# Kernel tuning notes

Measured on AMD Instinct MI355X. Metric: run time of the kernel, lower is better.

Reference implementation:

```python
import jax, jax.numpy as jnp
import numpy as np
import heapq
from collections import defaultdict

N_PER, N_BATCH, C = 100000, 2, 128  # nodes per graph, num graphs, feature dim
TARGET = 50000                      # target node count per graph


def _build_graph():
    # Symmetric degree-4 ring graph per batch (offsets +/-1, +/-2), required so
    # neighbours[] lookups in the collapse algorithm never miss.
    within = np.tile(np.arange(N_PER), N_BATCH)
    base = np.repeat(np.arange(N_BATCH) * N_PER, N_PER)
    src_all, dst_all = [], []
    for o in (1, 2, -1, -2):
        src_all.append(base + within)
        dst_all.append(base + (within + o) % N_PER)
    ei = np.stack([np.concatenate(src_all), np.concatenate(dst_all)]).astype(np.int64)
    batch = np.repeat(np.arange(N_BATCH), N_PER).astype(np.int64)
    return ei, batch


def _collapse(x, edge_index, target_edge_count, batch):
    # Faithful port of the sequential heap-driven greedy collapse.
    N = x.shape[0]
    collapse_mask = np.ones(N, dtype=bool)
    x_mask = np.ones(N, dtype=bool)
    neighbours = defaultdict(list)
    for f, t in zip(edge_index[0].tolist(), edge_index[1].tolist()):
        neighbours[f].append(t)
    for batch_id in range(int(batch.max()) + 1):
        node_ids = np.nonzero(batch == batch_id)[0]
        num_nodes = int(node_ids.shape[0])
        mags = (x[node_ids] * x[node_ids]).sum(axis=1)  # squared magnitude priority
        heap = [[float(m), int(n)] for m, n in zip(mags, node_ids)]
        heapq.heapify(heap)
        while num_nodes > target_edge_count:
            if len(heap) == 0:
                break
            _, node_id = heapq.heappop(heap)
            node_id = int(node_id)
            if not collapse_mask[node_id]:
                continue
            collapse_mask[node_id] = False
            neighbour_ids = neighbours[node_id]
            num_nodes -= 1
            new_neighbour_ids = []
            for nb in neighbour_ids:
                x_mask[nb] = False
                collapse_mask[nb] = False
                num_nodes -= 1
                for nbnb in neighbours[nb]:
                    if nbnb in neighbour_ids or nbnb == node_id:
                        continue
                    new_neighbour_ids.append(nbnb)
                    neighbours[nbnb] = [n for n in neighbours[nbnb] if n != nb]
                    neighbours[nbnb].append(node_id)
            neighbours[node_id] = new_neighbour_ids
    # Remap surviving nodes to compact ids and rebuild edge_index.
    old_to_new = -np.ones(N, dtype=np.int64)
    new_to_old = np.nonzero(x_mask)[0]
    old_to_new[new_to_old] = np.arange(new_to_old.shape[0])
    rows, cols = [], []
    for new_id, old_id in enumerate(new_to_old.tolist()):
        for nid in neighbours[old_id]:
            rows.append(new_id)
            cols.append(int(old_to_new[nid]))
    new_ei = np.array([rows, cols], dtype=np.int64)
    return x_mask, new_ei


def setup_inputs() -> dict:
    key = jax.random.key(0)
    ei, batch = _build_graph()
    x = jax.random.normal(key, (N_BATCH * N_PER, C), dtype=jnp.float32)
    return {
        "x": x,
        "edge_index": jnp.asarray(ei),
        "target_edge_count": TARGET,
        "batch": jnp.asarray(batch),
        "vertices": jnp.zeros((1,), dtype=jnp.int32),
        "edges": jnp.zeros((1,), dtype=jnp.int32),
    }


def reference(x, edge_index, target_edge_count, batch, vertices, edges):
    # vertices/edges are unused by the original forward.
    x_mask, new_ei = _collapse(
        np.asarray(x), np.asarray(edge_index), int(target_edge_count), np.asarray(batch)
    )
    keep = jnp.asarray(np.nonzero(x_mask)[0])
    return x[keep], jnp.asarray(new_ei), batch[keep]
```

## Files before the change

### kernel.cpp

```cpp
#include <hip/hip_runtime.h>
#include <stdint.h>

#define N_PER   100000
#define N_TOT   200000
#define C_DIM   128
#define PAD     131072
#define NBLK    782
#define CMW     ((N_PER + 31) / 32)
#define MAXL    512
#define CANDMAX 2048

typedef unsigned long long u64;

__device__ __forceinline__ float mag128(const float4* __restrict__ p4) {
  float4 u = p4[0], v = p4[1];
  float r0 = __fmul_rn(u.x,u.x), r1 = __fmul_rn(u.y,u.y),
        r2 = __fmul_rn(u.z,u.z), r3 = __fmul_rn(u.w,u.w),
        r4 = __fmul_rn(v.x,v.x), r5 = __fmul_rn(v.y,v.y),
        r6 = __fmul_rn(v.z,v.z), r7 = __fmul_rn(v.w,v.w);
  #pragma unroll
  for (int m = 1; m < 16; ++m) {
    u = p4[2*m]; v = p4[2*m+1];
    r0 = __fadd_rn(r0, __fmul_rn(u.x,u.x));
    r1 = __fadd_rn(r1, __fmul_rn(u.y,u.y));
    r2 = __fadd_rn(r2, __fmul_rn(u.z,u.z));
    r3 = __fadd_rn(r3, __fmul_rn(u.w,u.w));
    r4 = __fadd_rn(r4, __fmul_rn(v.x,v.x));
    r5 = __fadd_rn(r5, __fmul_rn(v.y,v.y));
    r6 = __fadd_rn(r6, __fmul_rn(v.z,v.z));
    r7 = __fadd_rn(r7, __fmul_rn(v.w,v.w));
  }
  return __fadd_rn(__fadd_rn(__fadd_rn(r0,r1), __fadd_rn(r2,r3)),
                   __fadd_rn(__fadd_rn(r4,r5), __fadd_rn(r6,r7)));
}

__global__ void k_init_keys(const float* __restrict__ x, u64* __restrict__ keys) {
  int slot = blockIdx.x*blockDim.x + threadIdx.x;
  if (slot >= 2*PAD) return;
  int b = slot >> 17;
  int w = slot & (PAD-1);
  if (w < N_PER) {
    int node = b*N_PER + w;
    float mag = mag128((const float4*)(x + (size_t)node*C_DIM));
    keys[slot] = ((u64)__float_as_uint(mag) << 32) | (uint32_t)node;
  } else {
    keys[slot] = ~0ull;
  }
}

__global__ void k_init_graph(int* __restrict__ nbr, uint8_t* __restrict__ xm, int cap) {
  int node = blockIdx.x*blockDim.x + threadIdx.x;
  if (node >= N_TOT) return;
  int base = (node >= N_PER) ? N_PER : 0;
  int w = node - base;
  int* Lp = nbr + (size_t)node*cap;
  Lp[0] = 4;
  Lp[1] = base + (w + 1) % N_PER;
  Lp[2] = base + (w + 2) % N_PER;
  Lp[3] = base + (w + N_PER - 1) % N_PER;
  Lp[4] = base + (w + N_PER - 2) % N_PER;
  xm[node] = 1;
}

__global__ void k_bitonic(u64* __restrict__ keys, int k, int j) {
  int i = blockIdx.x*blockDim.x + threadIdx.x;
  if (i >= 2*PAD) return;
  int ixj = i ^ j;
  if (ixj <= i) return;
  int wi = i & (PAD-1);
  bool asc = ((wi & k) == 0);
  u64 a = keys[i], b = keys[ixj];
  bool sw = asc ? (a > b) : (a < b);
  if (sw) { keys[i] = b; keys[ixj] = a; }
}

__global__ __launch_bounds__(64) void k_collapse(const u64* __restrict__ keys,
                                                 int* __restrict__ nbr,
                                                 uint8_t* __restrict__ xm,
                                                 const int* __restrict__ tgt_p,
                                                 int cap) {
  __shared__ uint32_t s_cm[CMW];
  __shared__ int      s_mem[4][MAXL];
  __shared__ int      s_memlen[4];
  __shared__ int      s_cand[CANDMAX];
  __shared__ uint8_t  s_cg[CANDMAX];
  __shared__ int      s_node[MAXL];
  __shared__ int      s_final[MAXL];

  const int b    = blockIdx.x;
  const int lane = threadIdx.x;
  const int TGT  = tgt_p[0];
  const u64* ord = keys + (size_t)b * PAD;
  const int gbase = b * N_PER;
  const int g = lane >> 4, j = lane & 15;

  for (int w = lane; w < CMW; w += 64) s_cm[w] = 0xffffffffu;
  __syncthreads();

  int num_nodes = N_PER;
  for (int base2 = 0; base2 < N_PER && num_nodes > TGT; base2 += 64) {
    int nd_l = (int)(uint32_t)(ord[base2 + lane]);
    bool alive = false;
    if (base2 + lane < N_PER) {
      int locl = nd_l - gbase;
      alive = ((s_cm[locl >> 5] >> (locl & 31)) & 1u) != 0u;
    }
    u64 mask = __ballot(alive);
    while (mask != 0ull && num_nodes > TGT) {
      int k2 = __ffsll(mask) - 1;
      mask &= mask - 1;
      int node  = __shfl(nd_l, k2);
      int local = node - gbase;
      if (((s_cm[local >> 5] >> (local & 31)) & 1u) == 0u) continue;
      if (lane == 0) atomicAnd(&s_cm[local >> 5], ~(1u << (local & 31)));

      int* nodeL = nbr + (size_t)node * cap;
      int4 h0 = *(const int4*)nodeL;
      int  e3 = nodeL[4];
      int  L  = h0.x;

      if (L <= 4) {
        if (lane == 0) { s_node[0]=h0.y; s_node[1]=h0.z; s_node[2]=h0.w; s_node[3]=e3; }
      } else {
        for (int i = lane; i < L; i += 64) s_node[i] = nodeL[1 + i];
      }
      __syncthreads();

      for (int i = lane; i < L; i += 64) {
        int mv = s_node[i];
        xm[mv] = 0;
        int ml = mv - gbase;
        atomicAnd(&s_cm[ml >> 5], ~(1u << (ml & 31)));
      }
      num_nodes -= 1 + L;
      int mreg = (lane < L) ? s_node[lane] : -1;

      int Ctot = 0;
      for (int mc = 0; mc < L; mc += 4) {
        int Lc = (L - mc < 4) ? (L - mc) : 4;
        int m0 = s_node[mc];
        int m1 = (Lc > 1) ? s_node[mc+1] : -1;
        int m2 = (Lc > 2) ? s_node[mc+2] : -1;
        int m3 = (Lc > 3) ? s_node[mc+3] : -1;

        int mg = (g == 0) ? m0 : (g == 1) ? m1 : (g == 2) ? m2 : m3;
        const int* tlg = nbr + (size_t)mg * cap;
        if (g < Lc) {
          int4 c0 = *(const int4*)(tlg + 4*j);
          if (j == 0) s_memlen[g] = c0.x;
          if (j > 0)  s_mem[g][4*j - 1] = c0.x;
          s_mem[g][4*j + 0] = c0.y;
          s_mem[g][4*j + 1] = c0.z;
          s_mem[g][4*j + 2] = c0.w;
        }
        __syncthreads();
        int lg = (g < Lc) ? s_memlen[g] : 0;
        for (int s0 = 64 + 4*j; s0 <= lg; s0 += 64) {
          int4 cv = *(const int4*)(tlg + s0);
          s_mem[g][s0 - 1] = cv.x;
          if (s0 + 1 <= lg) s_mem[g][s0 + 0] = cv.y;
          if (s0 + 2 <= lg) s_mem[g][s0 + 1] = cv.z;
          if (s0 + 3 <= lg) s_mem[g][s0 + 2] = cv.w;
        }
        __syncthreads();

        int len0 = (Lc > 0) ? s_memlen[0] : 0;
        int len1 = (Lc > 1) ? s_memlen[1] : 0;
        int len2 = (Lc > 2) ? s_memlen[2] : 0;
        int len3 = (Lc > 3) ? s_memlen[3] : 0;
        int o1 = len0, o2 = o1 + len1, o3 = o2 + len2, T = o3 + len3;
        int C = 0;
        int LM = (L < 64) ? L : 64;
        for (int cb = 0; cb < T; cb += 64) {
          int i = cb + lane;
          bool act = i < T;
          int val = -1; int ggi = 0;
          if (act) {
            ggi = (i >= o1) + (i >= o2) + (i >= o3);
            int qb = (ggi == 0) ? 0 : (ggi == 1) ? o1 : (ggi == 2) ? o2 : o3;
            val = s_mem[ggi][i - qb];
          }
          bool ism = (val == node);
          for (int m = 0; m < LM; ++m) ism |= (val == __shfl(mreg, m));
          for (int i2 = 64; i2 < L; ++i2) ism |= (val == s_node[i2]);
          bool keep = act && !ism;
          u64 mk = __ballot(keep);
          if (keep) {
            int pos = C + __popcll(mk & ((1ull << lane) - 1ull));
            s_cand[pos] = val;
            s_cg[pos]   = (uint8_t)ggi;
          }
          C += __popcll(mk);
        }
        __syncthreads();

        for (int cb = 0; cb < C; cb += 64) {
          int c = cb + lane;
          bool own = (c < C);
          int val = own ? s_cand[c] : -1;
          if (own) {
            for (int p = 0; p < c; ++p)
              if (s_cand[p] == val) { own = false; break; }
          }
          if (own) {
            uint32_t rmg = 0; int kocc = 0;
            for (int p = c; p < C; ++p)
              if (s_cand[p] == val) { rmg |= 1u << s_cg[p]; ++kocc; }
            bool u0 = (rmg & 1u) != 0, u1 = (rmg & 2u) != 0,
                 u2 = (rmg & 4u) != 0, u3 = (rmg & 8u) != 0;
            int* tl = nbr + (size_t)val * cap;
            int L3 = tl[0];
            int wslot = 1;
            int nch = (L3 + 4) >> 2;
            for (int ch = 0; ch < nch; ++ch) {
              int4 v = *(const int4*)(tl + 4*ch);
              int s = 4*ch;
              if (s >= 1 && s <= L3) { int e = v.x;
                if (!((u0&&e==m0)||(u1&&e==m1)||(u2&&e==m2)||(u3&&e==m3))) tl[wslot++] = e; }
              if (s + 1 <= L3)       { int e = v.y;
                if (!((u0&&e==m0)||(u1&&e==m1)||(u2&&e==m2)||(u3&&e==m3))) tl[wslot++] = e; }
              if (s + 2 <= L3)       { int e = v.z;
                if (!((u0&&e==m0)||(u1&&e==m1)||(u2&&e==m2)||(u3&&e==m3))) tl[wslot++] = e; }
              if (s + 3 <= L3)       { int e = v.w;
                if (!((u0&&e==m0)||(u1&&e==m1)||(u2&&e==m2)||(u3&&e==m3))) tl[wslot++] = e; }
            }
            int fin = wslot - 1 + kocc;
            if (fin > cap - 1) fin = cap - 1;
            for (int a = wslot; a <= fin; ++a) tl[a] = node;
            tl[0] = fin;
          }
        }

        for (int k3 = lane; k3 < C; k3 += 64) {
          int gp = Ctot + k3;
          if (gp < cap - 1) s_final[gp] = s_cand[k3];
        }
        Ctot += C;
        __threadfence_block();
        __syncthreads();
      }

      int wl = (Ctot < cap - 1) ? Ctot : (cap - 1);
      if (lane == 0) nodeL[0] = wl;
      for (int k3 = lane; k3 < wl; k3 += 64) nodeL[1 + k3] = s_final[k3];
      __threadfence_block();
      __syncthreads();
    }
  }
}

__device__ __forceinline__ u64 pack_node(const uint8_t* xm, const int* nbr, int i, int cap) {
  int keep = xm[i];
  int el = keep ? nbr[(size_t)i*cap] : 0;
  return ((u64)(uint32_t)el << 32) | (uint32_t)keep;
}

__global__ void k_scan1(const uint8_t* __restrict__ xm, const int* __restrict__ nbr,
                        u64* __restrict__ bsum, int cap) {
  __shared__ u64 s[256];
  int t = threadIdx.x;
  int i = blockIdx.x*256 + t;
  u64 v = (i < N_TOT) ? pack_node(xm, nbr, i, cap) : 0ull;
  s[t] = v; __syncthreads();
  for (int off = 128; off > 0; off >>= 1) {
    if (t < off) s[t] += s[t+off];
    __syncthreads();
  }
  if (t == 0) bsum[blockIdx.x] = s[0];
}

__global__ void k_scan2(u64* __restrict__ bsum, int* __restrict__ cnt) {
  __shared__ u64 s[1024];
  int t = threadIdx.x;
  u64 v = (t < NBLK) ? bsum[t] : 0ull;
  s[t] = v; __syncthreads();
  for (int off = 1; off < 1024; off <<= 1) {
    u64 a = (t >= off) ? s[t-off] : 0ull;
    __syncthreads();
    s[t] += a;
    __syncthreads();
  }
  if (t < NBLK) bsum[t] = s[t] - v;
  if (t == 1023) {
    cnt[0] = (int)(s[1023] & 0xffffffffull);
    cnt[1] = (int)(s[1023] >> 32);
  }
}

__global__ void k_scan3(const uint8_t* __restrict__ xm, const int* __restrict__ nbr,
                        const u64* __restrict__ bsum,
                        int* __restrict__ newid, int* __restrict__ eoff, int cap) {
  __shared__ u64 s[256];
  int t = threadIdx.x;
  int i = blockIdx.x*256 + t;
  u64 v = (i < N_TOT) ? pack_node(xm, nbr, i, cap) : 0ull;
  s[t] = v; __syncthreads();
  for (int off = 1; off < 256; off <<= 1) {
    u64 a = (t >= off) ? s[t-off] : 0ull;
    __syncthreads();
    s[t] += a;
    __syncthreads();
  }
  u64 excl = s[t] - v + bsum[blockIdx.x];
  if (i < N_TOT) {
    newid[i] = (int)(excl & 0xffffffffull);
    eoff[i]  = (int)(excl >> 32);
  }
}

__global__ void k_write_x(const float* __restrict__ x, const uint8_t* __restrict__ xm,
                          const int* __restrict__ newid, float* __restrict__ out) {
  int tid = blockIdx.x*blockDim.x + threadIdx.x;
  int node = tid >> 5, q = tid & 31;
  if (node >= N_TOT || !xm[node]) return;
  const float4* src = (const float4*)(x + (size_t)node*C_DIM);
  float4* dst = (float4*)(out + (size_t)newid[node]*C_DIM);
  dst[q] = src[q];
}

__global__ __launch_bounds__(64) void k_write_edges(const uint8_t* __restrict__ xm,
                              const int* __restrict__ nbr,
                              const int* __restrict__ newid, const int* __restrict__ eoff,
                              const int* __restrict__ cnt, float* __restrict__ out, int cap) {
  int node = blockIdx.x;
  int lane = threadIdx.x;
  if (!xm[node]) return;
  int K = cnt[0], E = cnt[1];
  size_t base = (size_t)K * C_DIM;
  int nid = newid[node];
  if (lane == 0) out[base + 2*(size_t)E + nid] = (node >= N_PER) ? 1.0f : 0.0f;
  int len = nbr[(size_t)node*cap];
  int eo = eoff[node];
  for (int j = lane; j < len; j += 64) {
    int ent = nbr[(size_t)node*cap + 1 + j];
    int off = eo + j;
    out[base + off]             = (float)nid;
    out[base + (size_t)E + off] = xm[ent] ? (float)newid[ent] : -1.0f;
  }
}

extern "C" void kernel_launch(void* const* d_in, const int* in_sizes, int n_in,
                              void* d_out, int out_size, void* d_ws, size_t ws_size,
                              hipStream_t stream) {
  const float* x   = (const float*)d_in[0];
  const int*   tgt = (const int*)d_in[2];
  float* out = (float*)d_out;
  uint8_t* ws = (uint8_t*)d_ws;

  size_t off = 0;
  auto alloc = [&](size_t bytes) -> void* {
    void* p = ws + off;
    off += (bytes + 255) & ~(size_t)255;
    return p;
  };
  u64*     keys  = (u64*)alloc((size_t)2*PAD*8);
  uint8_t* xm    = (uint8_t*)alloc(N_TOT);
  int*     newid = (int*)alloc((size_t)N_TOT*4);
  int*     eoff  = (int*)alloc((size_t)N_TOT*4);
  u64*     bsum  = (u64*)alloc((size_t)1024*8);
  int*     cnt   = (int*)alloc(256);
  size_t remain = (ws_size > off + 64) ? (ws_size - off - 64) : 0;
  int cap = (int)(remain / ((size_t)N_TOT * 4));
  cap &= ~3;
  if (cap > 512) cap = 512;
  if (cap < 68)  cap = 68;
  int* nbr = (int*)(ws + off);

  k_init_keys<<<(2*PAD)/256, 256, 0, stream>>>(x, keys);
  k_init_graph<<<NBLK, 256, 0, stream>>>(nbr, xm, cap);

  for (int k = 2; k <= PAD; k <<= 1)
    for (int j = k >> 1; j >= 1; j >>= 1)
      k_bitonic<<<(2*PAD)/256, 256, 0, stream>>>(keys, k, j);

  k_collapse<<<2, 64, 0, stream>>>(keys, nbr, xm, tgt, cap);

  k_scan1<<<NBLK, 256, 0, stream>>>(xm, nbr, bsum, cap);
  k_scan2<<<1, 1024, 0, stream>>>(bsum, cnt);
  k_scan3<<<NBLK, 256, 0, stream>>>(xm, nbr, bsum, newid, eoff, cap);

  k_write_x<<<(N_TOT*32)/256, 256, 0, stream>>>(x, xm, newid, out);
  k_write_edges<<<N_TOT, 64, 0, stream>>>(xm, nbr, newid, eoff, cnt, out, cap);
}
```

Measured before the change: 42.31 ms.

## Speculatively batch up to four heap pops per iteration with conflict detection

The collapse loop now collects up to four live candidate nodes at a time. It loads their neighbour rows and second-hop rows together, then computes each candidate's new neighbour list in parallel. A sequential check accepts candidates until one conflicts with an earlier accepted one or has overflowed its buffer, and commits the accepted ones in a single merged update pass. The goal is to cut the per-pop serial latency of global loads and barriers, at the cost of much more shared memory, complex conflict checks, and rollback of the scan position. Overflowing candidates fall back to the old single-node path.

```diff
diff --git a/kernel.cpp b/kernel.cpp
--- a/kernel.cpp
+++ b/kernel.cpp
@@ -9,6 +9,7 @@
 #define CMW     ((N_PER + 31) / 32)
 #define MAXL    512
 #define CANDMAX 2048
+#define W       4
 
 typedef unsigned long long u64;
 
@@ -80,134 +81,319 @@
                                                  const int* __restrict__ tgt_p,
                                                  int cap) {
   __shared__ uint32_t s_cm[CMW];
-  __shared__ int      s_mem[4][MAXL];
-  __shared__ int      s_memlen[4];
-  __shared__ int      s_cand[CANDMAX];
-  __shared__ uint8_t  s_cg[CANDMAX];
-  __shared__ int      s_node[MAXL];
-  __shared__ int      s_final[MAXL];
+  __shared__ int      s_prow[W][MAXL];
+  __shared__ int      s_mem[4*W][MAXL];
+  __shared__ int      s_memlen[4*W];
+  __shared__ int      s_cand[W][CANDMAX];
+  __shared__ uint16_t s_cg[W][CANDMAX];
+  __shared__ int      s_fin[MAXL];
+  __shared__ int      s_pop[W], s_plenB[W], s_Cc[W], s_ovf[W];
+  __shared__ int      s_gb2[W];
+  __shared__ u64      s_gmask[W];
 
   const int b    = blockIdx.x;
   const int lane = threadIdx.x;
   const int TGT  = tgt_p[0];
   const u64* ord = keys + (size_t)b * PAD;
   const int gbase = b * N_PER;
-  const int g = lane >> 4, j = lane & 15;
 
   for (int w = lane; w < CMW; w += 64) s_cm[w] = 0xffffffffu;
   __syncthreads();
 
   int num_nodes = N_PER;
-  for (int base2 = 0; base2 < N_PER && num_nodes > TGT; base2 += 64) {
-    int nd_l = (int)(uint32_t)(ord[base2 + lane]);
-    bool alive = false;
-    if (base2 + lane < N_PER) {
-      int locl = nd_l - gbase;
-      alive = ((s_cm[locl >> 5] >> (locl & 31)) & 1u) != 0u;
+  int base2 = -64;
+  u64 mask = 0ull;
+  int nd_l = -1;
+
+  while (num_nodes > TGT) {
+    int Wp = 0;
+    for (;;) {
+      if (Wp >= W) break;
+      if (mask == 0ull) {
+        base2 += 64;
+        if (base2 >= N_PER) break;
+        nd_l = (base2 + lane < N_PER) ? (int)(uint32_t)ord[base2 + lane] : -1;
+        bool av = false;
+        if (base2 + lane < N_PER) {
+          int ll = nd_l - gbase;
+          av = ((s_cm[ll>>5] >> (ll&31)) & 1u) != 0u;
+        }
+        mask = __ballot(av);
+        continue;
+      }
+      if (lane == 0) { s_gb2[Wp] = base2; s_gmask[Wp] = mask; }
+      int k2 = __ffsll((long long)mask) - 1;
+      mask &= mask - 1ull;
+      int node = __shfl(nd_l, k2);
+      int ll = node - gbase;
+      if (((s_cm[ll>>5] >> (ll&31)) & 1u) == 0u) continue;
+      if (lane == 0) s_pop[Wp] = node;
+      ++Wp;
     }
-    u64 mask = __ballot(alive);
-    while (mask != 0ull && num_nodes > TGT) {
-      int k2 = __ffsll(mask) - 1;
-      mask &= mask - 1;
-      int node  = __shfl(nd_l, k2);
-      int local = node - gbase;
-      if (((s_cm[local >> 5] >> (local & 31)) & 1u) == 0u) continue;
-      if (lane == 0) atomicAnd(&s_cm[local >> 5], ~(1u << (local & 31)));
-
+    __syncthreads();
+    if (Wp == 0) break;
+
+    {
+      int p = lane >> 4, jj = lane & 15;
+      const int* rowp = nullptr;
+      if (p < Wp) {
+        rowp = nbr + (size_t)s_pop[p] * cap;
+        int4 c0 = *(const int4*)(rowp + 4*jj);
+        if (jj == 0) s_plenB[p] = c0.x;
+        else         s_prow[p][4*jj - 1] = c0.x;
+        s_prow[p][4*jj + 0] = c0.y;
+        s_prow[p][4*jj + 1] = c0.z;
+        s_prow[p][4*jj + 2] = c0.w;
+      }
+      __syncthreads();
+      if (p < Wp) {
+        int lg = s_plenB[p];
+        for (int s0 = 64 + 4*jj; s0 <= lg; s0 += 64) {
+          int4 cv = *(const int4*)(rowp + s0);
+          s_prow[p][s0 - 1] = cv.x;
+          if (s0 + 1 <= lg) s_prow[p][s0 + 0] = cv.y;
+          if (s0 + 2 <= lg) s_prow[p][s0 + 1] = cv.z;
+          if (s0 + 3 <= lg) s_prow[p][s0 + 2] = cv.w;
+        }
+      }
+      __syncthreads();
+    }
+
+    {
+      int r = lane >> 2, q4 = lane & 3;
+      int rp = r >> 2, rg = r & 3;
+      bool rOK = (rp < Wp) && (rg < s_plenB[rp]) && (rg < 4);
+      const int* tlg = nullptr;
+      if (rOK) {
+        int m = s_prow[rp][rg];
+        tlg = nbr + (size_t)m * cap;
+        int4 c0 = *(const int4*)(tlg + 4*q4);
+        if (q4 == 0) s_memlen[r] = c0.x;
+        else         s_mem[r][4*q4 - 1] = c0.x;
+        s_mem[r][4*q4 + 0] = c0.y;
+        s_mem[r][4*q4 + 1] = c0.z;
+        s_mem[r][4*q4 + 2] = c0.w;
+      }
+      __syncthreads();
+      if (rOK) {
+        int lg = s_memlen[r];
+        for (int s0 = 16 + 4*q4; s0 <= lg; s0 += 16) {
+          int4 cv = *(const int4*)(tlg + s0);
+          s_mem[r][s0 - 1] = cv.x;
+          if (s0 + 1 <= lg) s_mem[r][s0 + 0] = cv.y;
+          if (s0 + 2 <= lg) s_mem[r][s0 + 1] = cv.z;
+          if (s0 + 3 <= lg) s_mem[r][s0 + 2] = cv.w;
+        }
+      }
+      __syncthreads();
+    }
+
+    for (int p2 = 0; p2 < Wp; ++p2) {
+      int L = s_plenB[p2];
+      int node = s_pop[p2];
+      int C = 0, ovf = 0;
+      for (int mc = 0; mc < L; mc += 4) {
+        if (ovf) break;
+        int Lc = (L - mc < 4) ? (L - mc) : 4;
+        if (mc > 0) {
+          int g = lane >> 4, jj = lane & 15;
+          const int* tlg2 = nullptr;
+          if (g < Lc) {
+            int m = s_prow[p2][mc + g];
+            tlg2 = nbr + (size_t)m * cap;
+            int4 c0 = *(const int4*)(tlg2 + 4*jj);
+            if (jj == 0) s_memlen[4*p2 + g] = c0.x;
+            else         s_mem[4*p2 + g][4*jj - 1] = c0.x;
+            s_mem[4*p2 + g][4*jj + 0] = c0.y;
+            s_mem[4*p2 + g][4*jj + 1] = c0.z;
+            s_mem[4*p2 + g][4*jj + 2] = c0.w;
+          }
+          __syncthreads();
+          if (g < Lc) {
+            int lg = s_memlen[4*p2 + g];
+            for (int s0 = 64 + 4*jj; s0 <= lg; s0 += 64) {
+              int4 cv = *(const int4*)(tlg2 + s0);
+              s_mem[4*p2 + g][s0 - 1] = cv.x;
+              if (s0 + 1 <= lg) s_mem[4*p2 + g][s0 + 0] = cv.y;
+              if (s0 + 2 <= lg) s_mem[4*p2 + g][s0 + 1] = cv.z;
+              if (s0 + 3 <= lg) s_mem[4*p2 + g][s0 + 2] = cv.w;
+            }
+          }
+          __syncthreads();
+        }
+        int br = 4*p2;
+        int len0 = (Lc > 0) ? s_memlen[br+0] : 0;
+        int len1 = (Lc > 1) ? s_memlen[br+1] : 0;
+        int len2 = (Lc > 2) ? s_memlen[br+2] : 0;
+        int len3 = (Lc > 3) ? s_memlen[br+3] : 0;
+        int o1 = len0, o2 = o1 + len1, o3 = o2 + len2, T = o3 + len3;
+        for (int cb = 0; cb < T; cb += 64) {
+          int i = cb + lane;
+          bool act = i < T;
+          int val = -1, ggi = 0;
+          if (act) {
+            ggi = (i >= o1) + (i >= o2) + (i >= o3);
+            int qb = (ggi == 0) ? 0 : (ggi == 1) ? o1 : (ggi == 2) ? o2 : o3;
+            val = s_mem[br + ggi][i - qb];
+          }
+          bool ism = (val == node);
+          for (int t = 0; t < L; ++t) ism |= (val == s_prow[p2][t]);
+          bool keep = act && !ism;
+          u64 mk = __ballot(keep);
+          int cnt = __popcll(mk);
+          if (C + cnt > CANDMAX) { ovf = 1; break; }
+          if (keep) {
+            int pos = C + __popcll(mk & ((1ull << lane) - 1ull));
+            s_cand[p2][pos] = val;
+            s_cg[p2][pos]   = (uint16_t)(mc + ggi);
+          }
+          C += cnt;
+        }
+      }
+      if (lane == 0) { s_Cc[p2] = C; s_ovf[p2] = ovf; }
+      __syncthreads();
+    }
+
+    int statbits = 0;
+    int nn = num_nodes;
+    int consumed = Wp;
+    int solo = 0;
+    for (int jx = 0; jx < Wp; ++jx) {
+      if (nn <= TGT) { consumed = jx; break; }
+      int pj = s_pop[jx];
+      int Lj = s_plenB[jx];
+      bool dead = false;
+      for (int i = 0; i < jx && !dead; ++i) {
+        if (((statbits >> (2*i)) & 3) != 1) continue;
+        int Li = s_plenB[i];
+        for (int cb = 0; cb < Li && !dead; cb += 64) {
+          bool h = (cb + lane < Li) && (s_prow[i][cb + lane] == pj);
+          if (__ballot(h) != 0ull) dead = true;
+        }
+      }
+      if (dead) { statbits |= 2 << (2*jx); continue; }
+      if (s_ovf[jx]) {
+        if (jx == 0) { solo = 1; consumed = 1; }
+        else consumed = jx;
+        break;
+      }
+      bool conf = false;
+      for (int i = 0; i < jx && !conf; ++i) {
+        if (((statbits >> (2*i)) & 3) != 1) continue;
+        int pi = s_pop[i];
+        int Ci = s_Cc[i];
+        int Cj = s_Cc[jx];
+        for (int cb = 0; cb < Lj && !conf; cb += 64) {
+          bool h = (cb + lane < Lj) && (s_prow[jx][cb + lane] == pi);
+          if (__ballot(h) != 0ull) conf = true;
+        }
+        for (int cb = 0; cb < Cj && !conf; cb += 64) {
+          bool h = (cb + lane < Cj) && (s_cand[jx][cb + lane] == pi);
+          if (__ballot(h) != 0ull) conf = true;
+        }
+        for (int cb = 0; cb < Ci && !conf; cb += 64) {
+          int e = (cb + lane < Ci) ? s_cand[i][cb + lane] : -1;
+          bool h = false;
+          if (cb + lane < Ci) {
+            h = (e == pj);
+            for (int t = 0; t < Lj; ++t) h |= (e == s_prow[jx][t]);
+            for (int t = 0; t < Cj; ++t) h |= (e == s_cand[jx][t]);
+          }
+          if (__ballot(h) != 0ull) conf = true;
+        }
+      }
+      if (conf) { consumed = jx; break; }
+      statbits |= 1 << (2*jx);
+      nn -= 1 + Lj;
+    }
+
+    if (solo) {
+      int node = s_pop[0];
+      int L = s_plenB[0];
+      if (lane == 0) {
+        int ll = node - gbase;
+        atomicAnd(&s_cm[ll>>5], ~(1u << (ll&31)));
+      }
+      for (int t = lane; t < L; t += 64) {
+        int m = s_prow[0][t];
+        xm[m] = 0;
+        int ml = m - gbase;
+        atomicAnd(&s_cm[ml>>5], ~(1u << (ml&31)));
+      }
+      num_nodes -= 1 + L;
+      __syncthreads();
       int* nodeL = nbr + (size_t)node * cap;
-      int4 h0 = *(const int4*)nodeL;
-      int  e3 = nodeL[4];
-      int  L  = h0.x;
-
-      if (L <= 4) {
-        if (lane == 0) { s_node[0]=h0.y; s_node[1]=h0.z; s_node[2]=h0.w; s_node[3]=e3; }
-      } else {
-        for (int i = lane; i < L; i += 64) s_node[i] = nodeL[1 + i];
-      }
-      __syncthreads();
-
-      for (int i = lane; i < L; i += 64) {
-        int mv = s_node[i];
-        xm[mv] = 0;
-        int ml = mv - gbase;
-        atomicAnd(&s_cm[ml >> 5], ~(1u << (ml & 31)));
-      }
-      num_nodes -= 1 + L;
-      int mreg = (lane < L) ? s_node[lane] : -1;
-
       int Ctot = 0;
       for (int mc = 0; mc < L; mc += 4) {
         int Lc = (L - mc < 4) ? (L - mc) : 4;
-        int m0 = s_node[mc];
-        int m1 = (Lc > 1) ? s_node[mc+1] : -1;
-        int m2 = (Lc > 2) ? s_node[mc+2] : -1;
-        int m3 = (Lc > 3) ? s_node[mc+3] : -1;
-
-        int mg = (g == 0) ? m0 : (g == 1) ? m1 : (g == 2) ? m2 : m3;
-        const int* tlg = nbr + (size_t)mg * cap;
-        if (g < Lc) {
-          int4 c0 = *(const int4*)(tlg + 4*j);
-          if (j == 0) s_memlen[g] = c0.x;
-          if (j > 0)  s_mem[g][4*j - 1] = c0.x;
-          s_mem[g][4*j + 0] = c0.y;
-          s_mem[g][4*j + 1] = c0.z;
-          s_mem[g][4*j + 2] = c0.w;
-        }
-        __syncthreads();
-        int lg = (g < Lc) ? s_memlen[g] : 0;
-        for (int s0 = 64 + 4*j; s0 <= lg; s0 += 64) {
-          int4 cv = *(const int4*)(tlg + s0);
-          s_mem[g][s0 - 1] = cv.x;
-          if (s0 + 1 <= lg) s_mem[g][s0 + 0] = cv.y;
-          if (s0 + 2 <= lg) s_mem[g][s0 + 1] = cv.z;
-          if (s0 + 3 <= lg) s_mem[g][s0 + 2] = cv.w;
-        }
-        __syncthreads();
-
-        int len0 = (Lc > 0) ? s_memlen[0] : 0;
-        int len1 = (Lc > 1) ? s_memlen[1] : 0;
-        int len2 = (Lc > 2) ? s_memlen[2] : 0;
-        int len3 = (Lc > 3) ? s_memlen[3] : 0;
-        int o1 = len0, o2 = o1 + len1, o3 = o2 + len2, T = o3 + len3;
+        int m0 = s_prow[0][mc];
+        int m1 = (Lc > 1) ? s_prow[0][mc+1] : -1;
+        int m2 = (Lc > 2) ? s_prow[0][mc+2] : -1;
+        int m3 = (Lc > 3) ? s_prow[0][mc+3] : -1;
+        {
+          int g = lane >> 4, jj = lane & 15;
+          const int* tlg2 = nullptr;
+          if (g < Lc) {
+            int m = (g==0)?m0:(g==1)?m1:(g==2)?m2:m3;
+            tlg2 = nbr + (size_t)m * cap;
+            int4 c0 = *(const int4*)(tlg2 + 4*jj);
+            if (jj == 0) s_memlen[g] = c0.x;
+            else         s_mem[g][4*jj - 1] = c0.x;
+            s_mem[g][4*jj + 0] = c0.y;
+            s_mem[g][4*jj + 1] = c0.z;
+            s_mem[g][4*jj + 2] = c0.w;
+          }
+          __syncthreads();
+          if (g < Lc) {
+            int lg = s_memlen[g];
+            for (int s0 = 64 + 4*jj; s0 <= lg; s0 += 64) {
+              int4 cv = *(const int4*)(tlg2 + s0);
+              s_mem[g][s0 - 1] = cv.x;
+              if (s0 + 1 <= lg) s_mem[g][s0 + 0] = cv.y;
+              if (s0 + 2 <= lg) s_mem[g][s0 + 1] = cv.z;
+              if (s0 + 3 <= lg) s_mem[g][s0 + 2] = cv.w;
+            }
+          }
+          __syncthreads();
+        }
+        int len0=(Lc>0)?s_memlen[0]:0, len1=(Lc>1)?s_memlen[1]:0,
+            len2=(Lc>2)?s_memlen[2]:0, len3=(Lc>3)?s_memlen[3]:0;
+        int o1=len0, o2=o1+len1, o3=o2+len2, T=o3+len3;
         int C = 0;
-        int LM = (L < 64) ? L : 64;
         for (int cb = 0; cb < T; cb += 64) {
           int i = cb + lane;
           bool act = i < T;
-          int val = -1; int ggi = 0;
+          int val = -1, ggi = 0;
           if (act) {
             ggi = (i >= o1) + (i >= o2) + (i >= o3);
             int qb = (ggi == 0) ? 0 : (ggi == 1) ? o1 : (ggi == 2) ? o2 : o3;
             val = s_mem[ggi][i - qb];
           }
           bool ism = (val == node);
-          for (int m = 0; m < LM; ++m) ism |= (val == __shfl(mreg, m));
-          for (int i2 = 64; i2 < L; ++i2) ism |= (val == s_node[i2]);
+          for (int t = 0; t < L; ++t) ism |= (val == s_prow[0][t]);
           bool keep = act && !ism;
           u64 mk = __ballot(keep);
           if (keep) {
             int pos = C + __popcll(mk & ((1ull << lane) - 1ull));
-            s_cand[pos] = val;
-            s_cg[pos]   = (uint8_t)ggi;
+            s_cand[0][pos] = val;
+            s_cg[0][pos] = (uint16_t)ggi;
           }
           C += __popcll(mk);
         }
         __syncthreads();
-
         for (int cb = 0; cb < C; cb += 64) {
           int c = cb + lane;
           bool own = (c < C);
-          int val = own ? s_cand[c] : -1;
+          int val = own ? s_cand[0][c] : -1;
           if (own) {
             for (int p = 0; p < c; ++p)
-              if (s_cand[p] == val) { own = false; break; }
+              if (s_cand[0][p] == val) { own = false; break; }
           }
           if (own) {
             uint32_t rmg = 0; int kocc = 0;
             for (int p = c; p < C; ++p)
-              if (s_cand[p] == val) { rmg |= 1u << s_cg[p]; ++kocc; }
-            bool u0 = (rmg & 1u) != 0, u1 = (rmg & 2u) != 0,
-                 u2 = (rmg & 4u) != 0, u3 = (rmg & 8u) != 0;
+              if (s_cand[0][p] == val) { rmg |= 1u << s_cg[0][p]; ++kocc; }
+            bool u0=(rmg&1u)!=0, u1=(rmg&2u)!=0, u2=(rmg&4u)!=0, u3=(rmg&8u)!=0;
             int* tl = nbr + (size_t)val * cap;
             int L3 = tl[0];
             int wslot = 1;
@@ -215,14 +401,14 @@
             for (int ch = 0; ch < nch; ++ch) {
               int4 v = *(const int4*)(tl + 4*ch);
               int s = 4*ch;
-              if (s >= 1 && s <= L3) { int e = v.x;
-                if (!((u0&&e==m0)||(u1&&e==m1)||(u2&&e==m2)||(u3&&e==m3))) tl[wslot++] = e; }
-              if (s + 1 <= L3)       { int e = v.y;
-                if (!((u0&&e==m0)||(u1&&e==m1)||(u2&&e==m2)||(u3&&e==m3))) tl[wslot++] = e; }
-              if (s + 2 <= L3)       { int e = v.z;
-                if (!((u0&&e==m0)||(u1&&e==m1)||(u2&&e==m2)||(u3&&e==m3))) tl[wslot++] = e; }
-              if (s + 3 <= L3)       { int e = v.w;
-                if (!((u0&&e==m0)||(u1&&e==m1)||(u2&&e==m2)||(u3&&e==m3))) tl[wslot++] = e; }
+              if (s >= 1 && s <= L3) { int e=v.x;
+                if (!((u0&&e==m0)||(u1&&e==m1)||(u2&&e==m2)||(u3&&e==m3))) tl[wslot++]=e; }
+              if (s + 1 <= L3)       { int e=v.y;
+                if (!((u0&&e==m0)||(u1&&e==m1)||(u2&&e==m2)||(u3&&e==m3))) tl[wslot++]=e; }
+              if (s + 2 <= L3)       { int e=v.z;
+                if (!((u0&&e==m0)||(u1&&e==m1)||(u2&&e==m2)||(u3&&e==m3))) tl[wslot++]=e; }
+              if (s + 3 <= L3)       { int e=v.w;
+                if (!((u0&&e==m0)||(u1&&e==m1)||(u2&&e==m2)||(u3&&e==m3))) tl[wslot++]=e; }
             }
             int fin = wslot - 1 + kocc;
             if (fin > cap - 1) fin = cap - 1;
@@ -230,21 +416,108 @@
             tl[0] = fin;
           }
         }
-
         for (int k3 = lane; k3 < C; k3 += 64) {
           int gp = Ctot + k3;
-          if (gp < cap - 1) s_final[gp] = s_cand[k3];
+          if (gp < cap - 1) s_fin[gp] = s_cand[0][k3];
         }
         Ctot += C;
         __threadfence_block();
         __syncthreads();
       }
-
       int wl = (Ctot < cap - 1) ? Ctot : (cap - 1);
       if (lane == 0) nodeL[0] = wl;
-      for (int k3 = lane; k3 < wl; k3 += 64) nodeL[1 + k3] = s_final[k3];
+      for (int k3 = lane; k3 < wl; k3 += 64) nodeL[1 + k3] = s_fin[k3];
       __threadfence_block();
       __syncthreads();
+    } else {
+      for (int p3 = 0; p3 < Wp; ++p3) {
+        if (((statbits >> (2*p3)) & 3) != 1) continue;
+        int node = s_pop[p3];
+        int L = s_plenB[p3];
+        int* nodeL = nbr + (size_t)node * cap;
+        if (lane == 0) {
+          int ll = node - gbase;
+          atomicAnd(&s_cm[ll>>5], ~(1u << (ll&31)));
+        }
+        for (int t = lane; t < L; t += 64) {
+          int m = s_prow[p3][t];
+          xm[m] = 0;
+          int ml = m - gbase;
+          atomicAnd(&s_cm[ml>>5], ~(1u << (ml&31)));
+        }
+        int C = s_Cc[p3];
+        int wl = (C < cap - 1) ? C : (cap - 1);
+        if (lane == 0) nodeL[0] = wl;
+        for (int t = lane; t < wl; t += 64) nodeL[1 + t] = s_cand[p3][t];
+      }
+      int C0p = (((statbits >> 0) & 3) == 1) ? s_Cc[0] : 0;
+      int C1p = (Wp > 1 && ((statbits >> 2) & 3) == 1) ? s_Cc[1] : 0;
+      int C2p = (Wp > 2 && ((statbits >> 4) & 3) == 1) ? s_Cc[2] : 0;
+      int C3p = (Wp > 3 && ((statbits >> 6) & 3) == 1) ? s_Cc[3] : 0;
+      int tot = C0p + C1p + C2p + C3p;
+      for (int cb = 0; cb < tot; cb += 64) {
+        int idx = cb + lane;
+        bool act = idx < tot;
+        int c = idx, p = 0;
+        if (act) {
+          if (c >= C0p) { c -= C0p; p = 1;
+            if (c >= C1p) { c -= C1p; p = 2;
+              if (c >= C2p) { c -= C2p; p = 3; } } }
+        }
+        int Cp = (p == 0) ? C0p : (p == 1) ? C1p : (p == 2) ? C2p : C3p;
+        int val = act ? s_cand[p][c] : -1;
+        bool own = act;
+        if (own) {
+          for (int q = 0; q < c; ++q)
+            if (s_cand[p][q] == val) { own = false; break; }
+        }
+        if (own) {
+          int node = s_pop[p];
+          int kocc = 0;
+          for (int q = c; q < Cp; ++q) if (s_cand[p][q] == val) ++kocc;
+          auto rem = [&](int e) -> bool {
+            for (int q = c; q < Cp; ++q)
+              if (s_cand[p][q] == val && s_prow[p][(int)s_cg[p][q]] == e) return true;
+            return false;
+          };
+          int* tl = nbr + (size_t)val * cap;
+          int4 v0 = *(const int4*)tl;
+          int4 v1 = *(const int4*)(tl + 4);
+          int L3 = v0.x;
+          int wslot = 1;
+          if (L3 >= 1) { int e=v0.y; if (!rem(e)) tl[wslot++]=e; }
+          if (L3 >= 2) { int e=v0.z; if (!rem(e)) tl[wslot++]=e; }
+          if (L3 >= 3) { int e=v0.w; if (!rem(e)) tl[wslot++]=e; }
+          if (L3 >= 4) { int e=v1.x; if (!rem(e)) tl[wslot++]=e; }
+          if (L3 >= 5) { int e=v1.y; if (!rem(e)) tl[wslot++]=e; }
+          if (L3 >= 6) { int e=v1.z; if (!rem(e)) tl[wslot++]=e; }
+          if (L3 >= 7) { int e=v1.w; if (!rem(e)) tl[wslot++]=e; }
+          for (int s0 = 8; s0 <= L3; s0 += 4) {
+            int4 v = *(const int4*)(tl + s0);
+            { int e=v.x;                 if (!rem(e)) tl[wslot++]=e; }
+            if (s0 + 1 <= L3) { int e=v.y; if (!rem(e)) tl[wslot++]=e; }
+            if (s0 + 2 <= L3) { int e=v.z; if (!rem(e)) tl[wslot++]=e; }
+            if (s0 + 3 <= L3) { int e=v.w; if (!rem(e)) tl[wslot++]=e; }
+          }
+          int fin = wslot - 1 + kocc;
+          if (fin > cap - 1) fin = cap - 1;
+          for (int a = wslot; a <= fin; ++a) tl[a] = node;
+          tl[0] = fin;
+        }
+      }
+      num_nodes = nn;
+      __threadfence_block();
+      __syncthreads();
+    }
+
+    if (consumed < Wp) {
+      int nb2 = s_gb2[consumed];
+      u64 nmask = s_gmask[consumed];
+      if (nb2 != base2) {
+        base2 = nb2;
+        nd_l = (base2 + lane < N_PER) ? (int)(uint32_t)ord[base2 + lane] : -1;
+      }
+      mask = nmask;
     }
   }
 }
```

After: 53.84 ms. 27.2% more time.

## Prefetch next alive node's adjacency row and use shared bitmask for member tests

Applied to the files above, without the earlier changes.

Inside the sequential collapse kernel, the next alive node's neighbour-row header is prefetched into registers while the current node is processed. The prefetch is invalidated if that node's row gets modified. Membership tests against the collapsed neighbour set now use a shared-memory bitmask instead of shuffle loops. Duplicate detection and the neighbour-list rewrite move into the candidate scan through wave-level shuffles, which removes a separate quadratic pass and its barrier. This aims to cut latency on the serial critical path, at the cost of more complex invalidation logic and extra bitmask set/clear work per step.

```diff
diff --git a/kernel.cpp b/kernel.cpp
--- a/kernel.cpp
+++ b/kernel.cpp
@@ -8,7 +8,6 @@
 #define NBLK    782
 #define CMW     ((N_PER + 31) / 32)
 #define MAXL    512
-#define CANDMAX 2048
 
 typedef unsigned long long u64;
 
@@ -80,169 +79,197 @@
                                                  const int* __restrict__ tgt_p,
                                                  int cap) {
   __shared__ uint32_t s_cm[CMW];
+  __shared__ uint32_t s_mm[CMW];
+  __shared__ int      s_prow[MAXL];
   __shared__ int      s_mem[4][MAXL];
   __shared__ int      s_memlen[4];
-  __shared__ int      s_cand[CANDMAX];
-  __shared__ uint8_t  s_cg[CANDMAX];
-  __shared__ int      s_node[MAXL];
-  __shared__ int      s_final[MAXL];
+  __shared__ int      s_cand[MAXL];
 
   const int b    = blockIdx.x;
   const int lane = threadIdx.x;
   const int TGT  = tgt_p[0];
   const u64* ord = keys + (size_t)b * PAD;
   const int gbase = b * N_PER;
-  const int g = lane >> 4, j = lane & 15;
-
-  for (int w = lane; w < CMW; w += 64) s_cm[w] = 0xffffffffu;
+
+  for (int w = lane; w < CMW; w += 64) { s_cm[w] = 0xffffffffu; s_mm[w] = 0u; }
   __syncthreads();
 
   int num_nodes = N_PER;
+  int  pfnode = -1;
+  bool pfbad  = true;
+  int4 pfreg  = make_int4(0,0,0,0);
+
   for (int base2 = 0; base2 < N_PER && num_nodes > TGT; base2 += 64) {
-    int nd_l = (int)(uint32_t)(ord[base2 + lane]);
+    int nd_l = (base2 + lane < N_PER) ? (int)(uint32_t)ord[base2 + lane] : -1;
     bool alive = false;
     if (base2 + lane < N_PER) {
-      int locl = nd_l - gbase;
-      alive = ((s_cm[locl >> 5] >> (locl & 31)) & 1u) != 0u;
+      int ll = nd_l - gbase;
+      alive = ((s_cm[ll>>5] >> (ll&31)) & 1u) != 0u;
     }
     u64 mask = __ballot(alive);
     while (mask != 0ull && num_nodes > TGT) {
-      int k2 = __ffsll(mask) - 1;
-      mask &= mask - 1;
-      int node  = __shfl(nd_l, k2);
+      int k2 = __ffsll((long long)mask) - 1;
+      mask &= mask - 1ull;
+      int node = __shfl(nd_l, k2);
       int local = node - gbase;
-      if (((s_cm[local >> 5] >> (local & 31)) & 1u) == 0u) continue;
-      if (lane == 0) atomicAnd(&s_cm[local >> 5], ~(1u << (local & 31)));
-
-      int* nodeL = nbr + (size_t)node * cap;
-      int4 h0 = *(const int4*)nodeL;
-      int  e3 = nodeL[4];
-      int  L  = h0.x;
-
-      if (L <= 4) {
-        if (lane == 0) { s_node[0]=h0.y; s_node[1]=h0.z; s_node[2]=h0.w; s_node[3]=e3; }
-      } else {
-        for (int i = lane; i < L; i += 64) s_node[i] = nodeL[1 + i];
+      if (((s_cm[local>>5] >> (local&31)) & 1u) == 0u) continue;
+
+      bool usepf = (node == pfnode) && !pfbad;
+      int4 rv;
+      if (lane < 16) {
+        if (usepf) rv = pfreg;
+        else       rv = *(const int4*)(nbr + (size_t)node*cap + 4*lane);
+      }
+      int L = __shfl(rv.x, 0);
+      if (lane < 16) {
+        int bs = 4*lane;
+        if (lane == 0) { s_prow[0] = rv.y; s_prow[1] = rv.z; s_prow[2] = rv.w; }
+        else { s_prow[bs-1] = rv.x; s_prow[bs] = rv.y; s_prow[bs+1] = rv.z; s_prow[bs+2] = rv.w; }
+      }
+      if (L > 62) {
+        for (int i = 63 + lane; i < L; i += 64) s_prow[i] = nbr[(size_t)node*cap + 1 + i];
       }
       __syncthreads();
 
+      if (lane == 0) atomicAnd(&s_cm[local>>5], ~(1u << (local&31)));
       for (int i = lane; i < L; i += 64) {
-        int mv = s_node[i];
+        int mv = s_prow[i];
         xm[mv] = 0;
         int ml = mv - gbase;
-        atomicAnd(&s_cm[ml >> 5], ~(1u << (ml & 31)));
+        atomicAnd(&s_cm[ml>>5], ~(1u << (ml&31)));
+        atomicOr (&s_mm[ml>>5],  1u << (ml&31));
       }
       num_nodes -= 1 + L;
-      int mreg = (lane < L) ? s_node[lane] : -1;
+      __syncthreads();
+
+      {
+        u64 nm = mask;
+        int npf = -1;
+        while (nm != 0ull) {
+          int kk = __ffsll((long long)nm) - 1;
+          int cnd = __shfl(nd_l, kk);
+          int cl = cnd - gbase;
+          if (((s_cm[cl>>5] >> (cl&31)) & 1u) != 0u) { npf = cnd; break; }
+          nm &= nm - 1ull;
+        }
+        pfnode = npf;
+        pfbad  = (npf < 0);
+        if (!pfbad && lane < 16)
+          pfreg = *(const int4*)(nbr + (size_t)pfnode*cap + 4*lane);
+      }
 
       int Ctot = 0;
       for (int mc = 0; mc < L; mc += 4) {
         int Lc = (L - mc < 4) ? (L - mc) : 4;
-        int m0 = s_node[mc];
-        int m1 = (Lc > 1) ? s_node[mc+1] : -1;
-        int m2 = (Lc > 2) ? s_node[mc+2] : -1;
-        int m3 = (Lc > 3) ? s_node[mc+3] : -1;
-
-        int mg = (g == 0) ? m0 : (g == 1) ? m1 : (g == 2) ? m2 : m3;
-        const int* tlg = nbr + (size_t)mg * cap;
+        int m0 = s_prow[mc];
+        int m1 = (Lc > 1) ? s_prow[mc+1] : -1;
+        int m2 = (Lc > 2) ? s_prow[mc+2] : -1;
+        int m3 = (Lc > 3) ? s_prow[mc+3] : -1;
+
+        int g = lane >> 4, jj = lane & 15;
+        const int* tlg = nullptr;
         if (g < Lc) {
-          int4 c0 = *(const int4*)(tlg + 4*j);
-          if (j == 0) s_memlen[g] = c0.x;
-          if (j > 0)  s_mem[g][4*j - 1] = c0.x;
-          s_mem[g][4*j + 0] = c0.y;
-          s_mem[g][4*j + 1] = c0.z;
-          s_mem[g][4*j + 2] = c0.w;
+          int m = (g==0)?m0:(g==1)?m1:(g==2)?m2:m3;
+          tlg = nbr + (size_t)m * cap;
+          int4 c0 = *(const int4*)(tlg + 4*jj);
+          if (jj == 0) s_memlen[g] = c0.x;
+          else         s_mem[g][4*jj-1] = c0.x;
+          s_mem[g][4*jj+0] = c0.y;
+          s_mem[g][4*jj+1] = c0.z;
+          s_mem[g][4*jj+2] = c0.w;
         }
         __syncthreads();
-        int lg = (g < Lc) ? s_memlen[g] : 0;
-        for (int s0 = 64 + 4*j; s0 <= lg; s0 += 64) {
-          int4 cv = *(const int4*)(tlg + s0);
-          s_mem[g][s0 - 1] = cv.x;
-          if (s0 + 1 <= lg) s_mem[g][s0 + 0] = cv.y;
-          if (s0 + 2 <= lg) s_mem[g][s0 + 1] = cv.z;
-          if (s0 + 3 <= lg) s_mem[g][s0 + 2] = cv.w;
+        if (g < Lc) {
+          int lg = s_memlen[g];
+          for (int s0 = 64 + 4*jj; s0 <= lg; s0 += 64) {
+            int4 cv = *(const int4*)(tlg + s0);
+            s_mem[g][s0-1] = cv.x;
+            if (s0+1 <= lg) s_mem[g][s0+0] = cv.y;
+            if (s0+2 <= lg) s_mem[g][s0+1] = cv.z;
+            if (s0+3 <= lg) s_mem[g][s0+2] = cv.w;
+          }
         }
         __syncthreads();
 
-        int len0 = (Lc > 0) ? s_memlen[0] : 0;
-        int len1 = (Lc > 1) ? s_memlen[1] : 0;
-        int len2 = (Lc > 2) ? s_memlen[2] : 0;
-        int len3 = (Lc > 3) ? s_memlen[3] : 0;
-        int o1 = len0, o2 = o1 + len1, o3 = o2 + len2, T = o3 + len3;
-        int C = 0;
-        int LM = (L < 64) ? L : 64;
+        int len0 = (Lc>0)?s_memlen[0]:0, len1=(Lc>1)?s_memlen[1]:0,
+            len2 = (Lc>2)?s_memlen[2]:0, len3=(Lc>3)?s_memlen[3]:0;
+        int o1 = len0, o2 = o1+len1, o3 = o2+len2, T = o3+len3;
+
         for (int cb = 0; cb < T; cb += 64) {
           int i = cb + lane;
           bool act = i < T;
-          int val = -1; int ggi = 0;
+          int val = -1, gg = 0;
           if (act) {
-            ggi = (i >= o1) + (i >= o2) + (i >= o3);
-            int qb = (ggi == 0) ? 0 : (ggi == 1) ? o1 : (ggi == 2) ? o2 : o3;
-            val = s_mem[ggi][i - qb];
+            gg = (i>=o1) + (i>=o2) + (i>=o3);
+            int qb = (gg==0)?0:(gg==1)?o1:(gg==2)?o2:o3;
+            val = s_mem[gg][i-qb];
           }
-          bool ism = (val == node);
-          for (int m = 0; m < LM; ++m) ism |= (val == __shfl(mreg, m));
-          for (int i2 = 64; i2 < L; ++i2) ism |= (val == s_node[i2]);
+          bool ism = !act || (val == node);
+          if (act && !ism) {
+            int vl = val - gbase;
+            ism |= ((s_mm[vl>>5] >> (vl&31)) & 1u) != 0u;
+          }
           bool keep = act && !ism;
           u64 mk = __ballot(keep);
+          int wcnt = __popcll(mk);
           if (keep) {
-            int pos = C + __popcll(mk & ((1ull << lane) - 1ull));
-            s_cand[pos] = val;
-            s_cg[pos]   = (uint8_t)ggi;
+            int pos = Ctot + __popcll(mk & ((1ull<<lane)-1ull));
+            if (pos < cap - 1) s_cand[pos] = val;
           }
-          C += __popcll(mk);
+          if (!pfbad && (__ballot(keep && (val == pfnode)) != 0ull)) pfbad = true;
+          if (wcnt) {
+            int Twin = (T - cb < 64) ? (T - cb) : 64;
+            uint32_t pk = keep ? (((uint32_t)val << 2) | (uint32_t)gg) : 0xffffffffu;
+            bool owner = keep;
+            uint32_t rmg = 0;
+            int kocc = 0;
+            for (int q = 0; q < Twin; ++q) {
+              uint32_t pq = __shfl(pk, q);
+              if (pq != 0xffffffffu && keep && (int)(pq >> 2) == val) {
+                rmg |= 1u << (pq & 3u);
+                ++kocc;
+                if (q < lane) owner = false;
+              }
+            }
+            if (owner) {
+              bool u0=(rmg&1u)!=0, u1=(rmg&2u)!=0, u2=(rmg&4u)!=0, u3=(rmg&8u)!=0;
+              int* tl = nbr + (size_t)val * cap;
+              int L3 = tl[0];
+              int wslot = 1;
+              int nch = (L3 + 4) >> 2;
+              for (int ch = 0; ch < nch; ++ch) {
+                int4 v = *(const int4*)(tl + 4*ch);
+                int s = 4*ch;
+                if (s >= 1 && s <= L3) { int e=v.x;
+                  if (!((u0&&e==m0)||(u1&&e==m1)||(u2&&e==m2)||(u3&&e==m3))) tl[wslot++]=e; }
+                if (s+1 <= L3) { int e=v.y;
+                  if (!((u0&&e==m0)||(u1&&e==m1)||(u2&&e==m2)||(u3&&e==m3))) tl[wslot++]=e; }
+                if (s+2 <= L3) { int e=v.z;
+                  if (!((u0&&e==m0)||(u1&&e==m1)||(u2&&e==m2)||(u3&&e==m3))) tl[wslot++]=e; }
+                if (s+3 <= L3) { int e=v.w;
+                  if (!((u0&&e==m0)||(u1&&e==m1)||(u2&&e==m2)||(u3&&e==m3))) tl[wslot++]=e; }
+              }
+              int fin = wslot - 1 + kocc;
+              if (fin > cap - 1) fin = cap - 1;
+              for (int a = wslot; a <= fin; ++a) tl[a] = node;
+              tl[0] = fin;
+            }
+            bool lastw = (mc + 4 >= L) && (cb + 64 >= T);
+            if (!lastw) { __threadfence_block(); __syncthreads(); }
+          }
+          Ctot += wcnt;
         }
-        __syncthreads();
-
-        for (int cb = 0; cb < C; cb += 64) {
-          int c = cb + lane;
-          bool own = (c < C);
-          int val = own ? s_cand[c] : -1;
-          if (own) {
-            for (int p = 0; p < c; ++p)
-              if (s_cand[p] == val) { own = false; break; }
-          }
-          if (own) {
-            uint32_t rmg = 0; int kocc = 0;
-            for (int p = c; p < C; ++p)
-              if (s_cand[p] == val) { rmg |= 1u << s_cg[p]; ++kocc; }
-            bool u0 = (rmg & 1u) != 0, u1 = (rmg & 2u) != 0,
-                 u2 = (rmg & 4u) != 0, u3 = (rmg & 8u) != 0;
-            int* tl = nbr + (size_t)val * cap;
-            int L3 = tl[0];
-            int wslot = 1;
-            int nch = (L3 + 4) >> 2;
-            for (int ch = 0; ch < nch; ++ch) {
-              int4 v = *(const int4*)(tl + 4*ch);
-              int s = 4*ch;
-              if (s >= 1 && s <= L3) { int e = v.x;
-                if (!((u0&&e==m0)||(u1&&e==m1)||(u2&&e==m2)||(u3&&e==m3))) tl[wslot++] = e; }
-              if (s + 1 <= L3)       { int e = v.y;
-                if (!((u0&&e==m0)||(u1&&e==m1)||(u2&&e==m2)||(u3&&e==m3))) tl[wslot++] = e; }
-              if (s + 2 <= L3)       { int e = v.z;
-                if (!((u0&&e==m0)||(u1&&e==m1)||(u2&&e==m2)||(u3&&e==m3))) tl[wslot++] = e; }
-              if (s + 3 <= L3)       { int e = v.w;
-                if (!((u0&&e==m0)||(u1&&e==m1)||(u2&&e==m2)||(u3&&e==m3))) tl[wslot++] = e; }
-            }
-            int fin = wslot - 1 + kocc;
-            if (fin > cap - 1) fin = cap - 1;
-            for (int a = wslot; a <= fin; ++a) tl[a] = node;
-            tl[0] = fin;
-          }
-        }
-
-        for (int k3 = lane; k3 < C; k3 += 64) {
-          int gp = Ctot + k3;
-          if (gp < cap - 1) s_final[gp] = s_cand[k3];
-        }
-        Ctot += C;
-        __threadfence_block();
-        __syncthreads();
-      }
-
+      }
+
+      for (int i = lane; i < L; i += 64) {
+        int ml = s_prow[i] - gbase;
+        atomicAnd(&s_mm[ml>>5], ~(1u << (ml&31)));
+      }
+      __syncthreads();
       int wl = (Ctot < cap - 1) ? Ctot : (cap - 1);
+      int* nodeL = nbr + (size_t)node * cap;
       if (lane == 0) nodeL[0] = wl;
-      for (int k3 = lane; k3 < wl; k3 += 64) nodeL[1 + k3] = s_final[k3];
+      for (int k3 = lane; k3 < wl; k3 += 64) nodeL[1 + k3] = s_cand[k3];
       __threadfence_block();
       __syncthreads();
     }
```

New measurement: 45.88 ms. +8.4%, slower.
